# Optimization experiments

Measured on AMD Instinct MI355X. Metric: run time of the kernel, lower is better.

## Reference

```python
import jax, jax.numpy as jnp
import numpy as np

SP_BETA = 1.0       # rendering_options.sp_beta
INF_DELTA = 1e10    # use_inf_depth=True -> last delta is 1e10
EPS = 1e-10


def setup_inputs() -> dict:
    key = jax.random.key(0)
    k1, k2, k3 = jax.random.split(key, 3)
    B, R, S, C = 8, 16384, 64, 3  # batch, rays, samples-per-ray, rgb channels
    colors = jax.random.normal(k1, (B, R, S, C), dtype=jnp.float32)
    densities = jax.random.normal(k2, (B, R, S, 1), dtype=jnp.float32)
    # depths must be sorted (increasing) along the sample dimension
    depths = jnp.sort(
        jax.random.uniform(k3, (B, R, S, 1), dtype=jnp.float32, minval=0.1, maxval=6.0),
        axis=2,
    )
    return {"colors": colors, "densities": densities, "depths": depths}


def reference(colors, densities, depths):
    # deltas between consecutive samples, last delta = 1e10 (infinite far plane)
    deltas = depths[:, :, 1:] - depths[:, :, :-1]                      # [B,R,S-1,1]
    deltas = jnp.concatenate(
        [deltas, jnp.full_like(deltas[:, :, :1], INF_DELTA)], axis=2)  # [B,R,S,1]

    # clamp_mode == 'softplus' with beta=1.0: softplus(x*beta)/beta
    dens = jax.nn.softplus(densities * SP_BETA) / SP_BETA              # [B,R,S,1]

    alphas = 1.0 - jnp.exp(-deltas * dens)                             # [B,R,S,1]

    # transmittance: cumulative product of (1-alpha), with leading ones
    trans = jnp.cumprod(1.0 - alphas + EPS, axis=2)                    # [B,R,S,1]
    trans = jnp.concatenate([jnp.ones_like(trans[:, :, :1]), trans], axis=2)  # [B,R,S+1,1]

    final_transmittance = trans[:, :, -1, 0]                           # [B,R]
    weights = alphas * trans[:, :, :-1]                                # [B,R,S,1]

    rgb_final = (weights * colors).sum(axis=2)                         # [B,R,C]
    depth = (weights * depths).sum(axis=2)                             # [B,R,1]
    return rgb_final, depth, weights, final_transmittance
```

## Files before the change

kernel.cpp:

```cpp
#include <hip/hip_runtime.h>

#define INF_DELTA 1e10f
#define RM_EPS 1e-10f
#define LOG2E 1.4426950408889634f

__device__ __forceinline__ float softplus_log2(float x) {
    const float q  = __builtin_amdgcn_exp2f(-__builtin_fabsf(x) * LOG2E);
    const float l2 = __builtin_amdgcn_logf(1.0f + q);
    return __builtin_fmaf(__builtin_fmaxf(x, 0.0f), LOG2E, l2);
}

__global__ __launch_bounds__(256) void raymarch_kernel(
    const float4* __restrict__ colors4,
    const float4* __restrict__ densities4,
    const float4* __restrict__ depths4,
    float* __restrict__ rgb_out,
    float* __restrict__ depth_out,
    float4* __restrict__ weights4,
    float* __restrict__ trans_out,
    int n_rays)
{
    const int lane = threadIdx.x & 63;
    const int sl   = lane & 15;
    const int ray  = blockIdx.x * 16 + (((int)threadIdx.x >> 6) << 2) + (lane >> 4);
    if (ray >= n_rays) return;

    const long vbase = (long)ray * 16 + sl;

    const float4 d4 = depths4[vbase];
    const float4 x4 = densities4[vbase];
    const float4* cp = colors4 + (long)ray * 48 + sl * 3;
    const float4 ca = cp[0], cb = cp[1], cc = cp[2];

    const float dnext = __shfl_down(d4.x, 1, 64);
    const float del0 = d4.y - d4.x;
    const float del1 = d4.z - d4.y;
    const float del2 = d4.w - d4.z;
    const float del3 = (sl == 15) ? INF_DELTA : (dnext - d4.w);

    const float y0 = __builtin_amdgcn_exp2f(-del0 * softplus_log2(x4.x));
    const float y1 = __builtin_amdgcn_exp2f(-del1 * softplus_log2(x4.y));
    const float y2 = __builtin_amdgcn_exp2f(-del2 * softplus_log2(x4.z));
    const float y3 = __builtin_amdgcn_exp2f(-del3 * softplus_log2(x4.w));

    const float t0 = y0 + RM_EPS, t1 = y1 + RM_EPS;
    const float t2 = y2 + RM_EPS, t3 = y3 + RM_EPS;

    const float p1 = t0, p2 = t0 * t1, p3 = p2 * t2;
    const float ptot = p3 * t3;

    float P = ptot;
    #pragma unroll
    for (int off = 1; off < 16; off <<= 1) {
        const float o = __shfl_up(P, off, 16);
        P *= (sl >= off) ? o : 1.0f;
    }
    float Pexcl = __shfl_up(P, 1, 16);
    if (sl == 0) Pexcl = 1.0f;
    const float finalT = __shfl(P, 15, 16);

    const float w0 = (1.0f - y0) * Pexcl;
    const float w1 = (1.0f - y1) * (Pexcl * p1);
    const float w2 = (1.0f - y2) * (Pexcl * p2);
    const float w3 = (1.0f - y3) * (Pexcl * p3);

    float4 wv; wv.x = w0; wv.y = w1; wv.z = w2; wv.w = w3;
    weights4[vbase] = wv;

    float s0 = w0*ca.x + w1*ca.w + w2*cb.z + w3*cc.y;
    float s1 = w0*ca.y + w1*cb.x + w2*cb.w + w3*cc.z;
    float s2 = w0*ca.z + w1*cb.y + w2*cc.x + w3*cc.w;
    float s3 = w0*d4.x + w1*d4.y + w2*d4.z + w3*d4.w;

    #pragma unroll
    for (int off = 1; off <= 2; off <<= 1) {
        s0 += __shfl_xor(s0, off, 16);
        s1 += __shfl_xor(s1, off, 16);
        s2 += __shfl_xor(s2, off, 16);
        s3 += __shfl_xor(s3, off, 16);
    }
    const int sel = sl & 3;
    float v = (sel == 0) ? s0 : (sel == 1) ? s1 : (sel == 2) ? s2 : s3;
    #pragma unroll
    for (int off = 4; off < 16; off <<= 1) {
        v += __shfl_xor(v, off, 16);
    }

    if (sl < 3) {
        rgb_out[(long)ray * 3 + sl] = v;
    } else if (sl == 3) {
        depth_out[ray] = v;
    } else if (sl == 4) {
        trans_out[ray] = finalT;
    }
}

extern "C" void kernel_launch(void* const* d_in, const int* in_sizes, int n_in,
                              void* d_out, int out_size, void* d_ws, size_t ws_size,
                              hipStream_t stream) {
    const float4* colors4    = (const float4*)d_in[0];
    const float4* densities4 = (const float4*)d_in[1];
    const float4* depths4    = (const float4*)d_in[2];

    const int n_rays = in_sizes[1] / 64;

    float* out      = (float*)d_out;
    float* rgb      = out;
    float* depth_o  = rgb + (long)n_rays * 3;
    float4* weights = (float4*)(depth_o + n_rays);
    float* trans    = (float*)(weights + (long)n_rays * 16);

    const int blocks = (n_rays + 15) / 16;
    raymarch_kernel<<<blocks, 256, 0, stream>>>(
        colors4, densities4, depths4, rgb, depth_o, weights, trans, n_rays);
}
```

Before: 201.4 us.

## Replace cross-lane shuffles with DPP row shifts for scans and reductions

The transmittance prefix product and the per-ray color/depth reductions now use DPP row_shr instructions instead of ds_bpermute-based shuffles. The weighted sums are restructured algebraically so the exclusive prefix is factored out, letting the local partial sums be computed before the scan. Weights are written with nontemporal stores, and a single lane writes all per-ray outputs. This removes LDS-permute latency, but the reduction now does 16 DPP adds instead of a mixed shuffle tree, and the depth neighbour fetch relies on DPP row semantics across 16-lane rows.

```diff
diff --git a/kernel.cpp b/kernel.cpp
--- a/kernel.cpp
+++ b/kernel.cpp
@@ -3,6 +3,16 @@
 #define INF_DELTA 1e10f
 #define RM_EPS 1e-10f
 #define LOG2E 1.4426950408889634f
+
+typedef float floatx4 __attribute__((ext_vector_type(4)));
+
+__device__ __forceinline__ int   f2i(float x){ union{float f;int i;}u; u.f=x; return u.i; }
+__device__ __forceinline__ float i2f(int x)  { union{int i;float f;}u; u.i=x; return u.f; }
+
+template<int CTRL>
+__device__ __forceinline__ float dpp_mov(float src, float old){
+    return i2f(__builtin_amdgcn_update_dpp(f2i(old), f2i(src), CTRL, 0xF, 0xF, false));
+}
 
 __device__ __forceinline__ float softplus_log2(float x) {
     const float q  = __builtin_amdgcn_exp2f(-__builtin_fabsf(x) * LOG2E);
@@ -20,9 +30,9 @@
     float* __restrict__ trans_out,
     int n_rays)
 {
-    const int lane = threadIdx.x & 63;
-    const int sl   = lane & 15;
-    const int ray  = blockIdx.x * 16 + (((int)threadIdx.x >> 6) << 2) + (lane >> 4);
+    const int tid = threadIdx.x;
+    const int sl  = tid & 15;
+    const int ray = blockIdx.x * 16 + (tid >> 4);
     if (ray >= n_rays) return;
 
     const long vbase = (long)ray * 16 + sl;
@@ -32,7 +42,7 @@
     const float4* cp = colors4 + (long)ray * 48 + sl * 3;
     const float4 ca = cp[0], cb = cp[1], cc = cp[2];
 
-    const float dnext = __shfl_down(d4.x, 1, 64);
+    const float dnext = dpp_mov<0x101>(d4.x, 0.0f);
     const float del0 = d4.y - d4.x;
     const float del1 = d4.z - d4.y;
     const float del2 = d4.w - d4.z;
@@ -46,52 +56,47 @@
     const float t0 = y0 + RM_EPS, t1 = y1 + RM_EPS;
     const float t2 = y2 + RM_EPS, t3 = y3 + RM_EPS;
 
-    const float p1 = t0, p2 = t0 * t1, p3 = p2 * t2;
-    const float ptot = p3 * t3;
+    const float ex1 = t0, ex2 = t0 * t1, ex3 = ex2 * t2;
+    const float ptot = ex3 * t3;
+
+    const float e0 = (1.0f - y0);
+    const float e1 = (1.0f - y1) * ex1;
+    const float e2 = (1.0f - y2) * ex2;
+    const float e3 = (1.0f - y3) * ex3;
+
+    float s0 = e0*ca.x + e1*ca.w + e2*cb.z + e3*cc.y;
+    float s1 = e0*ca.y + e1*cb.x + e2*cb.w + e3*cc.z;
+    float s2 = e0*ca.z + e1*cb.y + e2*cc.x + e3*cc.w;
+    float s3 = e0*d4.x + e1*d4.y + e2*d4.z + e3*d4.w;
 
     float P = ptot;
-    #pragma unroll
-    for (int off = 1; off < 16; off <<= 1) {
-        const float o = __shfl_up(P, off, 16);
-        P *= (sl >= off) ? o : 1.0f;
-    }
-    float Pexcl = __shfl_up(P, 1, 16);
-    if (sl == 0) Pexcl = 1.0f;
-    const float finalT = __shfl(P, 15, 16);
+    P *= dpp_mov<0x111>(P, 1.0f);
+    P *= dpp_mov<0x112>(P, 1.0f);
+    P *= dpp_mov<0x114>(P, 1.0f);
+    P *= dpp_mov<0x118>(P, 1.0f);
+    const float Pexcl = dpp_mov<0x111>(P, 1.0f);
 
-    const float w0 = (1.0f - y0) * Pexcl;
-    const float w1 = (1.0f - y1) * (Pexcl * p1);
-    const float w2 = (1.0f - y2) * (Pexcl * p2);
-    const float w3 = (1.0f - y3) * (Pexcl * p3);
+    floatx4 wv;
+    wv.x = e0 * Pexcl; wv.y = e1 * Pexcl; wv.z = e2 * Pexcl; wv.w = e3 * Pexcl;
+    __builtin_nontemporal_store(wv, (floatx4*)&weights4[vbase]);
 
-    float4 wv; wv.x = w0; wv.y = w1; wv.z = w2; wv.w = w3;
-    weights4[vbase] = wv;
+    float v0 = Pexcl * s0, v1 = Pexcl * s1, v2 = Pexcl * s2, v3 = Pexcl * s3;
+    v0 += dpp_mov<0x111>(v0, 0.0f); v0 += dpp_mov<0x112>(v0, 0.0f);
+    v0 += dpp_mov<0x114>(v0, 0.0f); v0 += dpp_mov<0x118>(v0, 0.0f);
+    v1 += dpp_mov<0x111>(v1, 0.0f); v1 += dpp_mov<0x112>(v1, 0.0f);
+    v1 += dpp_mov<0x114>(v1, 0.0f); v1 += dpp_mov<0x118>(v1, 0.0f);
+    v2 += dpp_mov<0x111>(v2, 0.0f); v2 += dpp_mov<0x112>(v2, 0.0f);
+    v2 += dpp_mov<0x114>(v2, 0.0f); v2 += dpp_mov<0x118>(v2, 0.0f);
+    v3 += dpp_mov<0x111>(v3, 0.0f); v3 += dpp_mov<0x112>(v3, 0.0f);
+    v3 += dpp_mov<0x114>(v3, 0.0f); v3 += dpp_mov<0x118>(v3, 0.0f);
 
-    float s0 = w0*ca.x + w1*ca.w + w2*cb.z + w3*cc.y;
-    float s1 = w0*ca.y + w1*cb.x + w2*cb.w + w3*cc.z;
-    float s2 = w0*ca.z + w1*cb.y + w2*cc.x + w3*cc.w;
-    float s3 = w0*d4.x + w1*d4.y + w2*d4.z + w3*d4.w;
-
-    #pragma unroll
-    for (int off = 1; off <= 2; off <<= 1) {
-        s0 += __shfl_xor(s0, off, 16);
-        s1 += __shfl_xor(s1, off, 16);
-        s2 += __shfl_xor(s2, off, 16);
-        s3 += __shfl_xor(s3, off, 16);
-    }
-    const int sel = sl & 3;
-    float v = (sel == 0) ? s0 : (sel == 1) ? s1 : (sel == 2) ? s2 : s3;
-    #pragma unroll
-    for (int off = 4; off < 16; off <<= 1) {
-        v += __shfl_xor(v, off, 16);
-    }
-
-    if (sl < 3) {
-        rgb_out[(long)ray * 3 + sl] = v;
-    } else if (sl == 3) {
-        depth_out[ray] = v;
-    } else if (sl == 4) {
-        trans_out[ray] = finalT;
+    if (sl == 15) {
+        const long r3 = (long)ray * 3;
+        rgb_out[r3 + 0] = v0;
+        rgb_out[r3 + 1] = v1;
+        rgb_out[r3 + 2] = v2;
+        depth_out[ray]  = v3;
+        trans_out[ray]  = P;
     }
 }
 
```

New measurement: 202.5 us. Within noise of the previous version (+0.5%).
